# Optimization experiments

Hardware: AMD Instinct MI355X
Metric: run time of the kernel (lower is better)

The kernel has to match this reference:

```python
import jax, jax.numpy as jnp
import numpy as np

DEPTH = 8
N_FEATURES = 512
N_CLASSES = 1000
N_LEAVES = 2 ** DEPTH          # 256
N_INTERNAL = N_LEAVES - 1      # 255
BATCH = 16384


def _path_tables():
    """Static routing tables for a complete binary tree (heap indexing).

    nodes[d, l] = internal node index visited at level d on the path to leaf l
    bits[d, l]  = 1 if path goes right at that node, else 0
    """
    leaves = np.arange(N_LEAVES)
    nodes = np.stack([(2 ** d - 1) + (leaves >> (DEPTH - d)) for d in range(DEPTH)])
    bits = np.stack([(leaves >> (DEPTH - 1 - d)) & 1 for d in range(DEPTH)])
    return nodes, bits


_NODES, _BITS = _path_tables()


def setup_inputs() -> dict:
    key = jax.random.key(0)
    k1, k2, k3 = jax.random.split(key, 3)
    x = jax.random.normal(k1, (BATCH, N_FEATURES), dtype=jnp.float32)
    # xavier-uniform-ish scale for the stacked gate weights
    gate_w = jax.random.normal(k2, (N_INTERNAL, N_FEATURES), dtype=jnp.float32) / np.sqrt(N_FEATURES)
    gate_b = jnp.zeros((N_INTERNAL,), dtype=jnp.float32)
    leaf_logits = jax.random.normal(k3, (N_LEAVES, N_CLASSES), dtype=jnp.float32) * 0.1
    return {"x": x, "gate_w": gate_w, "gate_b": gate_b, "leaf_logits": leaf_logits}


def reference(x, gate_w, gate_b, leaf_logits):
    # All internal-node gates as one batched matmul: [B, N_INTERNAL]
    p_right = jax.nn.sigmoid(jnp.einsum("bf,nf->bn", x, gate_w) + gate_b)
    # Arrival probability of each leaf: product of branch probs along its path.
    mu = jnp.ones((x.shape[0], N_LEAVES), dtype=x.dtype)
    for d in range(DEPTH):  # static loop over tree depth (8 iters)
        g = p_right[:, _NODES[d]]                       # [B, N_LEAVES]
        branch = jnp.where(_BITS[d] == 1, g, 1.0 - g)   # right vs left prob
        mu = mu * branch
    # Leaf class distributions: softmax per leaf over classes
    leaf_dists = jax.nn.softmax(leaf_logits, axis=-1)   # [N_LEAVES, N_CLASSES]
    return mu @ leaf_dists                              # [B, N_CLASSES]
```

## Files before the change

kernel.cpp:

```cpp
#include <hip/hip_runtime.h>

typedef __attribute__((ext_vector_type(8))) _Float16 f16x8;
typedef __attribute__((ext_vector_type(4))) _Float16 f16x4;
typedef __attribute__((ext_vector_type(4))) float   f32x4;

#define BATCH 16384
#define NFEAT 512
#define NCLS  1000
#define NLEAF 256
#define NINT  255
#define LDP   72
#define PSTR  257

__global__ __launch_bounds__(64) void cvt_gw(const float* __restrict__ gw,
                                             _Float16* __restrict__ gwF) {
  const int p = blockIdx.x;
  const int lane = threadIdx.x;
  const int c = (p >> 4) * 16 + (lane & 15);
  const int k0 = (p & 15) * 32 + (lane >> 4) * 8;
  f16x8 o = {};
  if (c < NINT) {
    float4 v0 = *(const float4*)&gw[(size_t)c * NFEAT + k0];
    float4 v1 = *(const float4*)&gw[(size_t)c * NFEAT + k0 + 4];
    o[0] = (_Float16)v0.x; o[1] = (_Float16)v0.y;
    o[2] = (_Float16)v0.z; o[3] = (_Float16)v0.w;
    o[4] = (_Float16)v1.x; o[5] = (_Float16)v1.y;
    o[6] = (_Float16)v1.z; o[7] = (_Float16)v1.w;
  }
  *(f16x8*)&gwF[((size_t)p * 64 + lane) * 8] = o;
}

__global__ __launch_bounds__(256) void softmax_t(const float* __restrict__ L,
                                                 _Float16* __restrict__ distF) {
  __shared__ float red[4];
  const int l = blockIdx.x, t = threadIdx.x;
  const int wave = t >> 6, lane = t & 63;
  const int kt = l >> 5, lhi_l = (l >> 3) & 3, jj = l & 7;
  float v[4];
  const bool live = t < 250;
  if (live) {
    float4 f = *(const float4*)&L[(size_t)l * NCLS + t * 4];
    v[0] = f.x; v[1] = f.y; v[2] = f.z; v[3] = f.w;
  } else {
    v[0] = v[1] = v[2] = v[3] = -1e30f;
  }
  float mx = fmaxf(fmaxf(v[0], v[1]), fmaxf(v[2], v[3]));
#pragma unroll
  for (int s = 32; s; s >>= 1) mx = fmaxf(mx, __shfl_xor(mx, s));
  if (lane == 0) red[wave] = mx;
  __syncthreads();
  mx = fmaxf(fmaxf(red[0], red[1]), fmaxf(red[2], red[3]));
  __syncthreads();
  float e[4], sum = 0.f;
#pragma unroll
  for (int i = 0; i < 4; ++i) { e[i] = __expf(v[i] - mx); sum += e[i]; }
  if (!live) { e[0] = e[1] = e[2] = e[3] = 0.f; sum = 0.f; }
#pragma unroll
  for (int s = 32; s; s >>= 1) sum += __shfl_xor(sum, s);
  if (lane == 0) red[wave] = sum;
  __syncthreads();
  sum = red[0] + red[1] + red[2] + red[3];
  float inv = 1.f / sum;
#pragma unroll
  for (int i = 0; i < 4; ++i) {
    int c = t * 4 + i;
    float val = live ? e[i] * inv : 0.f;
    int c16 = c >> 4, ln = c & 15;
    size_t idx = (((size_t)(c16 * 8 + kt)) * 64 + lhi_l * 16 + ln) * 8 + jj;
    distF[idx] = (_Float16)val;
  }
}

__global__ __launch_bounds__(512)
void g1mu(const float* __restrict__ x, const _Float16* __restrict__ gwF,
          const float* __restrict__ gb, _Float16* __restrict__ muFg) {
  __shared__ union {
    _Float16 A[32 * LDP];
    float P[32 * PSTR];
  } sm;

  const int tid  = threadIdx.x;
  const int wave = tid >> 6, lane = tid & 63;
  const int ln15 = lane & 15, lhi = lane >> 4;
  const int wr = wave >> 2, wc = wave & 3;
  const int r0 = blockIdx.x * 32;

  f32x4 acc1[4] = {};
  const int arow = tid >> 4, acol = (tid & 15) * 4;

  float4 pa = *(const float4*)&x[(size_t)(r0 + arow) * NFEAT + acol];
  for (int k = 0; k < NFEAT / 64; ++k) {
    {
      f16x4 h;
      h[0] = (_Float16)pa.x; h[1] = (_Float16)pa.y;
      h[2] = (_Float16)pa.z; h[3] = (_Float16)pa.w;
      *(f16x4*)&sm.A[arow * LDP + acol] = h;
    }
    __syncthreads();
    if (k < NFEAT / 64 - 1)
      pa = *(const float4*)&x[(size_t)(r0 + arow) * NFEAT + (k + 1) * 64 + acol];
#pragma unroll
    for (int kk = 0; kk < 2; ++kk) {
      f16x8 a = *(const f16x8*)&sm.A[(wr * 16 + ln15) * LDP + kk * 32 + lhi * 8];
#pragma unroll
      for (int n = 0; n < 4; ++n) {
        f16x8 b = *(const f16x8*)&gwF[(((size_t)(wc * 4 + n) * 16 + k * 2 + kk) * 64 + lane) * 8];
        acc1[n] = __builtin_amdgcn_mfma_f32_16x16x32_f16(a, b, acc1[n], 0, 0, 0);
      }
    }
    __syncthreads();
  }

#pragma unroll
  for (int n = 0; n < 4; ++n) {
    int col = wc * 64 + n * 16 + ln15;
    float bb = (col < NINT) ? gb[col] : 0.f;
#pragma unroll
    for (int j = 0; j < 4; ++j) {
      int rl = wr * 16 + lhi * 4 + j;
      float v = acc1[n][j] + bb;
      sm.P[rl * PSTR + col] = 1.f / (1.f + __expf(-v));
    }
  }
  __syncthreads();

  const int lf   = lane * 4;
  const int g_hi = lane >> 3;
  const int sub  = ((lane >> 1) & 3) * 16;
  const int j4   = (lane & 1) * 4;
#pragma unroll
  for (int rr = 0; rr < 4; ++rr) {
    int row = wave * 4 + rr;
    const float* p = &sm.P[row * PSTR];
    float pre = 1.f;
#pragma unroll
    for (int d = 0; d < 6; ++d) {
      int node = (1 << d) - 1 + (lf >> (8 - d));
      int bit  = (lf >> (7 - d)) & 1;
      float g = p[node];
      pre *= bit ? g : (1.f - g);
    }
    float g6  = p[63 + lane];
    float g7a = p[127 + 2 * lane];
    float g7b = p[128 + 2 * lane];
    f16x4 o;
    o[0] = (_Float16)(pre * (1.f - g6) * (1.f - g7a));
    o[1] = (_Float16)(pre * (1.f - g6) * g7a);
    o[2] = (_Float16)(pre * g6 * (1.f - g7b));
    o[3] = (_Float16)(pre * g6 * g7b);
    int row_g = r0 + row;
    size_t idx = (((size_t)(row_g >> 4) * 8 + g_hi) * 64 + sub + (row_g & 15)) * 8 + j4;
    *(f16x4*)&muFg[idx] = o;
  }
}

__global__ __launch_bounds__(256)
void g2(const _Float16* __restrict__ muFg, const _Float16* __restrict__ distF,
        float* __restrict__ out) {
  const int tid  = threadIdx.x;
  const int wave = tid >> 6, lane = tid & 63;
  const int ln15 = lane & 15, lhi = lane >> 4;
  const int row16 = blockIdx.x * 4 + wave;
  const int cs    = blockIdx.y;

  f16x8 aa[8];
#pragma unroll
  for (int kk = 0; kk < 8; ++kk)
    aa[kk] = *(const f16x8*)&muFg[(((size_t)row16 * 8 + kk) * 64 + lane) * 8];

  const int rb = row16 * 16 + lhi * 4;
  for (int ct = 0; ct < 16; ++ct) {
    const int c16 = cs * 16 + ct;
    f32x4 acc = {};
#pragma unroll
    for (int kk = 0; kk < 8; ++kk) {
      f16x8 bb = *(const f16x8*)&distF[(((size_t)c16 * 8 + kk) * 64 + lane) * 8];
      acc = __builtin_amdgcn_mfma_f32_16x16x32_f16(aa[kk], bb, acc, 0, 0, 0);
    }
    const int col = c16 * 16 + ln15;
    if (col < NCLS) {
#pragma unroll
      for (int j = 0; j < 4; ++j)
        out[(size_t)(rb + j) * NCLS + col] = acc[j];
    }
  }
}

extern "C" void kernel_launch(void* const* d_in, const int* in_sizes, int n_in,
                              void* d_out, int out_size, void* d_ws, size_t ws_size,
                              hipStream_t stream) {
  const float* x  = (const float*)d_in[0];
  const float* gw = (const float*)d_in[1];
  const float* gb = (const float*)d_in[2];
  const float* ll = (const float*)d_in[3];
  float* out = (float*)d_out;
  char* ws = (char*)d_ws;

  _Float16* gwF   = (_Float16*)(ws);
  _Float16* distF = (_Float16*)(ws + 262144);
  _Float16* muFg  = (_Float16*)(ws + 786432);

  cvt_gw   <<<256, 64,  0, stream>>>(gw, gwF);
  softmax_t<<<256, 256, 0, stream>>>(ll, distF);
  g1mu     <<<BATCH / 32, 512, 0, stream>>>(x, gwF, gb, muFg);
  g2       <<<dim3(BATCH / 64, 4), 256, 0, stream>>>(muFg, distF, out);
}
```

Baseline: 60.75 us.

## Double the gate-GEMM row tile, double-buffer LDS, and split the output GEMM finer

The gate/mu kernel now handles 64 rows per block instead of 32. Each wave computes two 16-row M tiles, so every gate-weight fragment loaded from global memory feeds two MFMAs. The x staging buffer in LDS is double-buffered, which removes one barrier per k-step and lets the next tile's global load overlap the MFMAs. The output GEMM grid doubles its column slices, each covering 8 class tiles, to expose more blocks. In exchange, the first kernel uses more LDS and launches half as many blocks, which lowers occupancy.

```diff
diff --git a/kernel.cpp b/kernel.cpp
--- a/kernel.cpp
+++ b/kernel.cpp
@@ -75,53 +75,72 @@
 void g1mu(const float* __restrict__ x, const _Float16* __restrict__ gwF,
           const float* __restrict__ gb, _Float16* __restrict__ muFg) {
   __shared__ union {
-    _Float16 A[32 * LDP];
-    float P[32 * PSTR];
+    _Float16 A[2][64 * LDP];
+    float P[64 * PSTR];
   } sm;
 
   const int tid  = threadIdx.x;
   const int wave = tid >> 6, lane = tid & 63;
   const int ln15 = lane & 15, lhi = lane >> 4;
   const int wr = wave >> 2, wc = wave & 3;
-  const int r0 = blockIdx.x * 32;
-
-  f32x4 acc1[4] = {};
+  const int r0 = blockIdx.x * 64;
+
+  f32x4 acc1[2][4] = {};
   const int arow = tid >> 4, acol = (tid & 15) * 4;
 
-  float4 pa = *(const float4*)&x[(size_t)(r0 + arow) * NFEAT + acol];
+  float4 pa, pa2;
+
+#define P1_LOAD(k0)                                                              \
+  {                                                                              \
+    pa  = *(const float4*)&x[(size_t)(r0 + arow) * NFEAT + (k0) + acol];         \
+    pa2 = *(const float4*)&x[(size_t)(r0 + 32 + arow) * NFEAT + (k0) + acol];    \
+  }
+#define P1_WRITE(buf)                                                            \
+  {                                                                              \
+    f16x4 h;                                                                     \
+    h[0] = (_Float16)pa.x; h[1] = (_Float16)pa.y;                                \
+    h[2] = (_Float16)pa.z; h[3] = (_Float16)pa.w;                                \
+    *(f16x4*)&sm.A[buf][arow * LDP + acol] = h;                                  \
+    h[0] = (_Float16)pa2.x; h[1] = (_Float16)pa2.y;                              \
+    h[2] = (_Float16)pa2.z; h[3] = (_Float16)pa2.w;                              \
+    *(f16x4*)&sm.A[buf][(32 + arow) * LDP + acol] = h;                           \
+  }
+
+  P1_LOAD(0);
+  P1_WRITE(0);
+  __syncthreads();
   for (int k = 0; k < NFEAT / 64; ++k) {
-    {
-      f16x4 h;
-      h[0] = (_Float16)pa.x; h[1] = (_Float16)pa.y;
-      h[2] = (_Float16)pa.z; h[3] = (_Float16)pa.w;
-      *(f16x4*)&sm.A[arow * LDP + acol] = h;
-    }
-    __syncthreads();
-    if (k < NFEAT / 64 - 1)
-      pa = *(const float4*)&x[(size_t)(r0 + arow) * NFEAT + (k + 1) * 64 + acol];
+    if (k < NFEAT / 64 - 1) P1_LOAD((k + 1) * 64);
 #pragma unroll
     for (int kk = 0; kk < 2; ++kk) {
-      f16x8 a = *(const f16x8*)&sm.A[(wr * 16 + ln15) * LDP + kk * 32 + lhi * 8];
+      f16x8 a[2];
+#pragma unroll
+      for (int m = 0; m < 2; ++m)
+        a[m] = *(const f16x8*)&sm.A[k & 1][(wr * 32 + m * 16 + ln15) * LDP + kk * 32 + lhi * 8];
 #pragma unroll
       for (int n = 0; n < 4; ++n) {
         f16x8 b = *(const f16x8*)&gwF[(((size_t)(wc * 4 + n) * 16 + k * 2 + kk) * 64 + lane) * 8];
-        acc1[n] = __builtin_amdgcn_mfma_f32_16x16x32_f16(a, b, acc1[n], 0, 0, 0);
+        acc1[0][n] = __builtin_amdgcn_mfma_f32_16x16x32_f16(a[0], b, acc1[0][n], 0, 0, 0);
+        acc1[1][n] = __builtin_amdgcn_mfma_f32_16x16x32_f16(a[1], b, acc1[1][n], 0, 0, 0);
       }
     }
+    if (k < NFEAT / 64 - 1) P1_WRITE((k + 1) & 1);
     __syncthreads();
   }
 
 #pragma unroll
-  for (int n = 0; n < 4; ++n) {
-    int col = wc * 64 + n * 16 + ln15;
-    float bb = (col < NINT) ? gb[col] : 0.f;
-#pragma unroll
-    for (int j = 0; j < 4; ++j) {
-      int rl = wr * 16 + lhi * 4 + j;
-      float v = acc1[n][j] + bb;
-      sm.P[rl * PSTR + col] = 1.f / (1.f + __expf(-v));
-    }
-  }
+  for (int m = 0; m < 2; ++m)
+#pragma unroll
+    for (int n = 0; n < 4; ++n) {
+      int col = wc * 64 + n * 16 + ln15;
+      float bb = (col < NINT) ? gb[col] : 0.f;
+#pragma unroll
+      for (int j = 0; j < 4; ++j) {
+        int rl = wr * 32 + m * 16 + lhi * 4 + j;
+        float v = acc1[m][n][j] + bb;
+        sm.P[rl * PSTR + col] = 1.f / (1.f + __expf(-v));
+      }
+    }
   __syncthreads();
 
   const int lf   = lane * 4;
@@ -129,8 +148,8 @@
   const int sub  = ((lane >> 1) & 3) * 16;
   const int j4   = (lane & 1) * 4;
 #pragma unroll
-  for (int rr = 0; rr < 4; ++rr) {
-    int row = wave * 4 + rr;
+  for (int rr = 0; rr < 8; ++rr) {
+    int row = wave * 8 + rr;
     const float* p = &sm.P[row * PSTR];
     float pre = 1.f;
 #pragma unroll
@@ -152,6 +171,8 @@
     size_t idx = (((size_t)(row_g >> 4) * 8 + g_hi) * 64 + sub + (row_g & 15)) * 8 + j4;
     *(f16x4*)&muFg[idx] = o;
   }
+#undef P1_LOAD
+#undef P1_WRITE
 }
 
 __global__ __launch_bounds__(256)
@@ -169,8 +190,8 @@
     aa[kk] = *(const f16x8*)&muFg[(((size_t)row16 * 8 + kk) * 64 + lane) * 8];
 
   const int rb = row16 * 16 + lhi * 4;
-  for (int ct = 0; ct < 16; ++ct) {
-    const int c16 = cs * 16 + ct;
+  for (int ct = 0; ct < 8; ++ct) {
+    const int c16 = cs * 8 + ct;
     f32x4 acc = {};
 #pragma unroll
     for (int kk = 0; kk < 8; ++kk) {
@@ -202,6 +223,6 @@
 
   cvt_gw   <<<256, 64,  0, stream>>>(gw, gwF);
   softmax_t<<<256, 256, 0, stream>>>(ll, distF);
-  g1mu     <<<BATCH / 32, 512, 0, stream>>>(x, gwF, gb, muFg);
-  g2       <<<dim3(BATCH / 64, 4), 256, 0, stream>>>(muFg, distF, out);
-}
+  g1mu     <<<BATCH / 64, 512, 0, stream>>>(x, gwF, gb, muFg);
+  g2       <<<dim3(BATCH / 64, 8), 256, 0, stream>>>(muFg, distF, out);
+}
```

Result: slower. 62.96 us (+3.6%).

## Stage mu tile in LDS and swap MFMA operands for vectorized output stores

Applied to the files above, without the earlier changes.

The g2 kernel now copies the block's 64-row mu tile into shared memory, and each wave owns four column tiles, holding their distF fragments in registers while reusing the shared mu tile across four row groups. The MFMA operands are swapped so the result is transposed, which lets each lane write four consecutive output columns as one 16-byte store instead of four strided scalar stores. This targets the scattered, uncoalesced fp32 output writes and the repeated distF reloads. It adds LDS traffic, a block barrier and more registers per wave.

```diff
diff --git a/kernel.cpp b/kernel.cpp
--- a/kernel.cpp
+++ b/kernel.cpp
@@ -157,31 +157,40 @@
 __global__ __launch_bounds__(256)
 void g2(const _Float16* __restrict__ muFg, const _Float16* __restrict__ distF,
         float* __restrict__ out) {
+  __shared__ _Float16 sMu[4 * 8 * 64 * 8];
   const int tid  = threadIdx.x;
   const int wave = tid >> 6, lane = tid & 63;
   const int ln15 = lane & 15, lhi = lane >> 4;
-  const int row16 = blockIdx.x * 4 + wave;
-  const int cs    = blockIdx.y;
-
-  f16x8 aa[8];
-#pragma unroll
-  for (int kk = 0; kk < 8; ++kk)
-    aa[kk] = *(const f16x8*)&muFg[(((size_t)row16 * 8 + kk) * 64 + lane) * 8];
-
-  const int rb = row16 * 16 + lhi * 4;
-  for (int ct = 0; ct < 16; ++ct) {
-    const int c16 = cs * 16 + ct;
-    f32x4 acc = {};
-#pragma unroll
-    for (int kk = 0; kk < 8; ++kk) {
-      f16x8 bb = *(const f16x8*)&distF[(((size_t)c16 * 8 + kk) * 64 + lane) * 8];
-      acc = __builtin_amdgcn_mfma_f32_16x16x32_f16(aa[kk], bb, acc, 0, 0, 0);
-    }
-    const int col = c16 * 16 + ln15;
-    if (col < NCLS) {
-#pragma unroll
-      for (int j = 0; j < 4; ++j)
-        out[(size_t)(rb + j) * NCLS + col] = acc[j];
+  const int bx = blockIdx.x;
+  const int by = blockIdx.y;
+
+  {
+    const f16x8* src = (const f16x8*)(muFg + (size_t)bx * 16384);
+    f16x8* dst = (f16x8*)sMu;
+#pragma unroll
+    for (int i = 0; i < 8; ++i)
+      dst[tid + i * 256] = src[tid + i * 256];
+  }
+  __syncthreads();
+
+  for (int h = 0; h < 4; ++h) {
+    const int c16 = by * 16 + wave * 4 + h;
+    f16x8 bb[8];
+#pragma unroll
+    for (int kk = 0; kk < 8; ++kk)
+      bb[kk] = *(const f16x8*)&distF[(((size_t)c16 * 8 + kk) * 64 + lane) * 8];
+#pragma unroll
+    for (int g = 0; g < 4; ++g) {
+      f32x4 acc = {};
+#pragma unroll
+      for (int kk = 0; kk < 8; ++kk) {
+        f16x8 aa = *(const f16x8*)&sMu[((g * 8 + kk) * 64 + lane) * 8];
+        acc = __builtin_amdgcn_mfma_f32_16x16x32_f16(bb[kk], aa, acc, 0, 0, 0);
+      }
+      const int brow = (bx * 4 + g) * 16 + ln15;
+      const int col4 = c16 * 16 + lhi * 4;
+      if (col4 < NCLS)
+        *(f32x4*)&out[(size_t)brow * NCLS + col4] = acc;
     }
   }
 }
```

After: 56.28 us. 1.08x faster.
